# Kernel tuning notes

Hardware: AMD Instinct MI355X
Metric: run time of the kernel (lower is better)

Reference implementation:

```python
import jax, jax.numpy as jnp
import numpy as np

C_IN, C_KEY, C_VAL, C_OUT = 256, 128, 128, 256
B, H, W = 4, 64, 64
BN_EPS = 1e-5


def conv1x1(x, w, b):
    # x: [B,C,H,W], w: [O,C], b: [O]
    return jnp.einsum('bchw,oc->bohw', x, w) + b[None, :, None, None]


def bn_relu(x, gamma, beta, mean, var):
    inv = jax.lax.rsqrt(var + BN_EPS)
    y = (x - mean[None, :, None, None]) * (gamma * inv)[None, :, None, None] + beta[None, :, None, None]
    return jax.nn.relu(y)


def setup_inputs() -> dict:
    key = jax.random.key(0)
    ks = jax.random.split(key, 16)
    s = 0.05
    return {
        'x_enc': jax.random.normal(ks[0], (B, C_IN, H, W), jnp.float32),
        'x_dec': jax.random.normal(ks[1], (B, C_IN, H, W), jnp.float32),
        # f_key: conv + BN params
        'wk': jax.random.normal(ks[2], (C_KEY, C_IN), jnp.float32) * s,
        'bk': jax.random.normal(ks[3], (C_KEY,), jnp.float32) * s,
        'gk': jax.random.uniform(ks[4], (C_KEY,), jnp.float32, 0.5, 1.5),
        'betak': jax.random.normal(ks[5], (C_KEY,), jnp.float32) * s,
        'mk': jax.random.normal(ks[6], (C_KEY,), jnp.float32) * s,
        'vk': jax.random.uniform(ks[7], (C_KEY,), jnp.float32, 0.5, 1.5),
        # f_query: conv + BN params
        'wq': jax.random.normal(ks[8], (C_KEY, C_IN), jnp.float32) * s,
        'bq': jax.random.normal(ks[9], (C_KEY,), jnp.float32) * s,
        'gq': jax.random.uniform(ks[10], (C_KEY,), jnp.float32, 0.5, 1.5),
        'betaq': jax.random.normal(ks[11], (C_KEY,), jnp.float32) * s,
        'mq': jax.random.normal(ks[12], (C_KEY,), jnp.float32) * s,
        'vq': jax.random.uniform(ks[13], (C_KEY,), jnp.float32, 0.5, 1.5),
        # f_value conv
        'wv': jax.random.normal(ks[14], (C_VAL, C_IN), jnp.float32) * s,
        'bv': jnp.zeros((C_VAL,), jnp.float32),
        # output projection W (random instead of zero-init to avoid degenerate baseline)
        'wo': jax.random.normal(ks[15], (C_OUT, C_VAL), jnp.float32) * s,
        'bo': jnp.zeros((C_OUT,), jnp.float32),
    }


def reference(x_enc, x_dec, wk, bk, gk, betak, mk, vk, wq, bq, gq, betaq, mq, vq, wv, bv, wo, bo):
    b, _, h, w = x_enc.shape
    hw = h * w
    # value: [B, HW, Cv]
    value = conv1x1(x_enc, wv, bv).reshape(b, C_VAL, hw).transpose(0, 2, 1)
    # query: [B, HW, Ck]
    query = bn_relu(conv1x1(x_dec, wq, bq), gq, betaq, mq, vq).reshape(b, C_KEY, hw).transpose(0, 2, 1)
    # key: [B, Ck, HW]
    key = bn_relu(conv1x1(x_enc, wk, bk), gk, betak, mk, vk).reshape(b, C_KEY, hw)
    sim = jnp.einsum('bqc,bck->bqk', query, key) * (C_KEY ** -0.5)  # [B, HW, HW]
    attn = jax.nn.softmax(sim, axis=-1)
    context = jnp.einsum('bqk,bkc->bqc', attn, value)  # [B, HW, Cv]
    context = context.transpose(0, 2, 1).reshape(b, C_VAL, h, w)
    return conv1x1(context, wo, bo)
```

## Files before the change

kernel.cpp:

```cpp
#include <hip/hip_runtime.h>

typedef __attribute__((ext_vector_type(8))) short short8;
typedef __attribute__((ext_vector_type(4))) float floatx4;

#define HW 4096
#define CIN 256
#define CK 128
#define COUT 256
#define NB 4
#define BN_EPS 1e-5f
#define SC2 0.12751744526f

#define MFMA(a, b, c) __builtin_amdgcn_mfma_f32_16x16x32_bf16((a), (b), (c), 0, 0, 0)

__device__ __forceinline__ unsigned short f2bf(float f) {
  union { float f; unsigned u; } v; v.f = f;
  unsigned r = v.u + 0x7fffu + ((v.u >> 16) & 1u);
  return (unsigned short)(r >> 16);
}

__device__ __forceinline__ short8 pack8(const float* p) {
  short8 r;
#pragma unroll
  for (int i = 0; i < 8; ++i) r[i] = (short)f2bf(p[i]);
  return r;
}

__global__ __launch_bounds__(256) void proj_kernel(
    const float* __restrict__ x_enc, const float* __restrict__ x_dec,
    const float* __restrict__ wq, const float* __restrict__ bq,
    const float* __restrict__ gq, const float* __restrict__ betaq,
    const float* __restrict__ mq, const float* __restrict__ vq,
    const float* __restrict__ wk, const float* __restrict__ bk,
    const float* __restrict__ gk, const float* __restrict__ betak,
    const float* __restrict__ mk, const float* __restrict__ vk,
    const float* __restrict__ wv, const float* __restrict__ bv,
    unsigned short* __restrict__ Qb, unsigned short* __restrict__ Kb,
    unsigned short* __restrict__ Vt)
{
  const int tid = threadIdx.x;
  const int pt = blockIdx.x;
  const int b  = blockIdx.y;
  const int pj = blockIdx.z;

  const float* X = (pj == 0) ? x_dec : x_enc;

  __shared__ float xF[64 * 68];
  __shared__ unsigned short xT[64 * 264];

  const float* Xs = X + (size_t)b * CIN * HW + (size_t)pt * 64;
#pragma unroll
  for (int qtr = 0; qtr < 4; ++qtr) {
    if (qtr) __syncthreads();
    {
      const int c = tid >> 2;
      const int p0 = (tid & 3) * 16;
      const float* src = Xs + (size_t)(qtr * 64 + c) * HW + p0;
#pragma unroll
      for (int j = 0; j < 4; ++j)
        *(float4*)&xF[c * 68 + p0 + j * 4] = *(const float4*)(src + j * 4);
    }
    __syncthreads();
    {
      const int p = tid & 63;
      const int cb = tid >> 6;
#pragma unroll
      for (int jj = 0; jj < 2; ++jj) {
        const int c0 = (jj * 4 + cb) * 8;
        float t[8];
#pragma unroll
        for (int u = 0; u < 8; ++u) t[u] = xF[(c0 + u) * 68 + p];
        *(short8*)&xT[p * 264 + qtr * 64 + c0] = pack8(t);
      }
    }
  }
  __syncthreads();

  const int wave = tid >> 6;
  const int lane = tid & 63;
  const int lane16 = lane & 15;
  const int quad = lane >> 4;

  if (pj == 0) {
    floatx4 acc[2][4];
#pragma unroll
    for (int mt = 0; mt < 2; ++mt)
#pragma unroll
      for (int nf = 0; nf < 4; ++nf) acc[mt][nf] = (floatx4){0.f, 0.f, 0.f, 0.f};

#pragma unroll
    for (int ks = 0; ks < 8; ++ks) {
      short8 af[2];
#pragma unroll
      for (int mt = 0; mt < 2; ++mt) {
        const int o = wave * 32 + mt * 16 + lane16;
        const float* Wr = wq + (size_t)o * CIN + ks * 32 + quad * 8;
        float t[8];
        *(float4*)(t) = *(const float4*)(Wr);
        *(float4*)(t + 4) = *(const float4*)(Wr + 4);
        af[mt] = pack8(t);
      }
#pragma unroll
      for (int nf = 0; nf < 4; ++nf) {
        const short8 bf = *(const short8*)&xT[(nf * 16 + lane16) * 264 + ks * 32 + quad * 8];
#pragma unroll
        for (int mt = 0; mt < 2; ++mt) acc[mt][nf] = MFMA(af[mt], bf, acc[mt][nf]);
      }
    }

    float sc[2][4], off[2][4];
#pragma unroll
    for (int mt = 0; mt < 2; ++mt)
#pragma unroll
      for (int r = 0; r < 4; ++r) {
        const int o = wave * 32 + mt * 16 + quad * 4 + r;
        const float s = gq[o] * rsqrtf(vq[o] + BN_EPS) * SC2;
        sc[mt][r] = s;
        off[mt][r] = (bq[o] - mq[o]) * s + betaq[o] * SC2;
      }
#pragma unroll
    for (int nf = 0; nf < 4; ++nf) {
      const size_t prow = ((size_t)b * HW + pt * 64 + nf * 16 + lane16) * CK;
#pragma unroll
      for (int mt = 0; mt < 2; ++mt) {
        ushort4 pk;
        pk.x = f2bf(fmaxf(acc[mt][nf][0] * sc[mt][0] + off[mt][0], 0.f));
        pk.y = f2bf(fmaxf(acc[mt][nf][1] * sc[mt][1] + off[mt][1], 0.f));
        pk.z = f2bf(fmaxf(acc[mt][nf][2] * sc[mt][2] + off[mt][2], 0.f));
        pk.w = f2bf(fmaxf(acc[mt][nf][3] * sc[mt][3] + off[mt][3], 0.f));
        *(ushort4*)(Qb + prow + wave * 32 + mt * 16 + quad * 4) = pk;
      }
    }
  } else {
    const bool isK = (wave < 2);
    floatx4 acc[4][4];
#pragma unroll
    for (int mt = 0; mt < 4; ++mt)
#pragma unroll
      for (int nf = 0; nf < 4; ++nf) acc[mt][nf] = (floatx4){0.f, 0.f, 0.f, 0.f};

#pragma unroll
    for (int ks = 0; ks < 8; ++ks) {
      short8 af[4];
#pragma unroll
      for (int mt = 0; mt < 4; ++mt) {
        const int o = wave * 64 + mt * 16 + lane16;
        const float* Wr = (isK ? wk + (size_t)o * CIN
                               : wv + (size_t)(o - 128) * CIN) + ks * 32 + quad * 8;
        float t[8];
        *(float4*)(t) = *(const float4*)(Wr);
        *(float4*)(t + 4) = *(const float4*)(Wr + 4);
        af[mt] = pack8(t);
      }
#pragma unroll
      for (int nf = 0; nf < 4; ++nf) {
        const short8 bf = *(const short8*)&xT[(nf * 16 + lane16) * 264 + ks * 32 + quad * 8];
#pragma unroll
        for (int mt = 0; mt < 4; ++mt) acc[mt][nf] = MFMA(af[mt], bf, acc[mt][nf]);
      }
    }

    if (isK) {
      float sc[4][4], off[4][4];
#pragma unroll
      for (int mt = 0; mt < 4; ++mt)
#pragma unroll
        for (int r = 0; r < 4; ++r) {
          const int o = wave * 64 + mt * 16 + quad * 4 + r;
          const float s = gk[o] * rsqrtf(vk[o] + BN_EPS);
          sc[mt][r] = s;
          off[mt][r] = (bk[o] - mk[o]) * s + betak[o];
        }
#pragma unroll
      for (int nf = 0; nf < 4; ++nf) {
        const size_t prow = ((size_t)b * HW + pt * 64 + nf * 16 + lane16) * CK;
#pragma unroll
        for (int mt = 0; mt < 4; ++mt) {
          ushort4 pk;
          pk.x = f2bf(fmaxf(acc[mt][nf][0] * sc[mt][0] + off[mt][0], 0.f));
          pk.y = f2bf(fmaxf(acc[mt][nf][1] * sc[mt][1] + off[mt][1], 0.f));
          pk.z = f2bf(fmaxf(acc[mt][nf][2] * sc[mt][2] + off[mt][2], 0.f));
          pk.w = f2bf(fmaxf(acc[mt][nf][3] * sc[mt][3] + off[mt][3], 0.f));
          *(ushort4*)(Kb + prow + wave * 64 + mt * 16 + quad * 4) = pk;
        }
      }
    } else {
#pragma unroll
      for (int mt = 0; mt < 4; ++mt) {
#pragma unroll
        for (int r = 0; r < 4; ++r) {
          const int c = wave * 64 + mt * 16 + quad * 4 + r - 128;
          const float bias = bv[c];
          unsigned short* dst = Vt + ((size_t)(b * CK + c)) * HW + pt * 64;
#pragma unroll
          for (int nf = 0; nf < 4; ++nf)
            dst[nf * 16 + lane16] = f2bf(acc[mt][nf][r] + bias);
        }
      }
    }
  }
}

template<int NKC>
__global__ __launch_bounds__(256, 2) void attn_kernel4(
    const unsigned short* __restrict__ Qb, const unsigned short* __restrict__ Kb,
    const unsigned short* __restrict__ Vt, float* __restrict__ Opart,
    float* __restrict__ Ml)
{
  constexpr int ITERS = 64 / NKC;
  const int tid = threadIdx.x;
  const int blk = blockIdx.x;
  const int b  = blk & 3;
  const int qt = (blk >> 2) & 31;
  const int kc = blk >> 7;

  const int wave = tid >> 6;
  const int lane = tid & 63;
  const int lane16 = lane & 15;
  const int quad = lane >> 4;

  __shared__ unsigned short Kl[64 * 136];
  __shared__ unsigned short Vl[128 * 72];
  __shared__ unsigned short Pl[4][32 * 72];
  unsigned short* Pw = &Pl[wave][0];

  const int q0 = qt * 128 + wave * 32;
  short8 qf[2][4];
  {
    const unsigned short* Qs = Qb + ((size_t)b * HW + q0) * CK;
#pragma unroll
    for (int mt = 0; mt < 2; ++mt)
#pragma unroll
      for (int ks = 0; ks < 4; ++ks)
        qf[mt][ks] = *(const short8*)(Qs + (size_t)(mt * 16 + lane16) * CK + ks * 32 + quad * 8);
  }

  short8 ones;
#pragma unroll
  for (int i = 0; i < 8; ++i) ones[i] = (short)0x3F80;

  floatx4 O[2][8];
  floatx4 Lacc[2];
#pragma unroll
  for (int mt = 0; mt < 2; ++mt) {
    Lacc[mt] = (floatx4){0.f, 0.f, 0.f, 0.f};
#pragma unroll
    for (int nf = 0; nf < 8; ++nf) O[mt][nf] = (floatx4){0.f, 0.f, 0.f, 0.f};
  }

  const int krow = tid >> 4;
  const int kcol = (tid & 15) * 8;
  const int vrow = tid >> 1;
  const int vcol = (tid & 1) * 32;

  const unsigned short* Kg = Kb + (size_t)b * HW * CK + (size_t)(kc * ITERS * 64) * CK;
  const unsigned short* Vg = Vt + (size_t)b * CK * HW + kc * ITERS * 64;

  short8 kr[4], vr[4];
#pragma unroll
  for (int i2 = 0; i2 < 4; ++i2)
    kr[i2] = *(const short8*)(Kg + (size_t)(krow + i2 * 16) * CK + kcol);
#pragma unroll
  for (int i2 = 0; i2 < 4; ++i2)
    vr[i2] = *(const short8*)(Vg + (size_t)vrow * HW + vcol + i2 * 8);

  for (int it = 0; it < ITERS; ++it) {
    __syncthreads();
#pragma unroll
    for (int i2 = 0; i2 < 4; ++i2)
      *(short8*)&Kl[(krow + i2 * 16) * 136 + kcol] = kr[i2];
#pragma unroll
    for (int i2 = 0; i2 < 4; ++i2)
      *(short8*)&Vl[vrow * 72 + vcol + i2 * 8] = vr[i2];
    __syncthreads();

    if (it + 1 < ITERS) {
      const unsigned short* Kn = Kg + (size_t)((it + 1) * 64) * CK;
      const unsigned short* Vn = Vg + (it + 1) * 64;
#pragma unroll
      for (int i2 = 0; i2 < 4; ++i2)
        kr[i2] = *(const short8*)(Kn + (size_t)(krow + i2 * 16) * CK + kcol);
#pragma unroll
      for (int i2 = 0; i2 < 4; ++i2)
        vr[i2] = *(const short8*)(Vn + (size_t)vrow * HW + vcol + i2 * 8);
    }

#pragma unroll
    for (int nf = 0; nf < 4; ++nf) {
      floatx4 s0 = (floatx4){0.f, 0.f, 0.f, 0.f};
      floatx4 s1 = (floatx4){0.f, 0.f, 0.f, 0.f};
#pragma unroll
      for (int ks = 0; ks < 4; ++ks) {
        const short8 kf = *(const short8*)&Kl[(nf * 16 + lane16) * 136 + ks * 32 + quad * 8];
        s0 = MFMA(qf[0][ks], kf, s0);
        s1 = MFMA(qf[1][ks], kf, s1);
      }
#pragma unroll
      for (int r = 0; r < 4; ++r) {
        Pw[(quad * 4 + r) * 72 + nf * 16 + lane16] =
            f2bf(__builtin_amdgcn_exp2f(s0[r]));
        Pw[(16 + quad * 4 + r) * 72 + nf * 16 + lane16] =
            f2bf(__builtin_amdgcn_exp2f(s1[r]));
      }
    }
    __threadfence_block();

#pragma unroll
    for (int ks = 0; ks < 2; ++ks) {
      const short8 pf0 = *(const short8*)&Pw[lane16 * 72 + ks * 32 + quad * 8];
      const short8 pf1 = *(const short8*)&Pw[(16 + lane16) * 72 + ks * 32 + quad * 8];
      Lacc[0] = MFMA(pf0, ones, Lacc[0]);
      Lacc[1] = MFMA(pf1, ones, Lacc[1]);
#pragma unroll
      for (int nf = 0; nf < 8; ++nf) {
        const short8 vf = *(const short8*)&Vl[(nf * 16 + lane16) * 72 + ks * 32 + quad * 8];
        O[0][nf] = MFMA(pf0, vf, O[0][nf]);
        O[1][nf] = MFMA(pf1, vf, O[1][nf]);
      }
    }
  }

  const int chunk = (b * 32 + qt) * NKC + kc;
  float* Op = Opart + (size_t)chunk * (128 * 128);
#pragma unroll
  for (int mt = 0; mt < 2; ++mt)
#pragma unroll
    for (int nf = 0; nf < 8; ++nf)
#pragma unroll
      for (int r = 0; r < 4; ++r)
        Op[(size_t)(wave * 32 + mt * 16 + quad * 4 + r) * 128 + nf * 16 + lane16] = O[mt][nf][r];
  if (lane16 == 0) {
    float* Mp = Ml + (size_t)chunk * 128 + wave * 32;
#pragma unroll
    for (int mt = 0; mt < 2; ++mt)
#pragma unroll
      for (int r = 0; r < 4; ++r)
        Mp[mt * 16 + quad * 4 + r] = Lacc[mt][r];
  }
}

template<int NKC>
__global__ __launch_bounds__(256) void outproj_kernel(
    const float* __restrict__ Opart, const float* __restrict__ Ml,
    const float* __restrict__ wo, const float* __restrict__ bo,
    float* __restrict__ out)
{
  const int tid = threadIdx.x;
  const int pt = blockIdx.x;
  const int b  = blockIdx.y;
  const int wave = tid >> 6;
  const int lane = tid & 63;
  const int lane16 = lane & 15;
  const int quad = lane >> 4;

  const int qt = pt >> 2;
  const int q0 = (pt & 3) * 32;
  const int chunk0 = (b * 32 + qt) * NKC;

  float invl[2];
#pragma unroll
  for (int nf = 0; nf < 2; ++nf) {
    const int qrow = q0 + nf * 16 + lane16;
    float L = 0.f;
#pragma unroll
    for (int k = 0; k < NKC; ++k) L += Ml[(size_t)(chunk0 + k) * 128 + qrow];
    invl[nf] = 1.f / L;
  }

  floatx4 acc[4][2];
#pragma unroll
  for (int mt = 0; mt < 4; ++mt)
#pragma unroll
    for (int nf = 0; nf < 2; ++nf) acc[mt][nf] = (floatx4){0.f, 0.f, 0.f, 0.f};

#pragma unroll
  for (int ks = 0; ks < 4; ++ks) {
    short8 af[4];
#pragma unroll
    for (int mt = 0; mt < 4; ++mt) {
      const int o = wave * 64 + mt * 16 + lane16;
      const float* Wr = wo + (size_t)o * CK + ks * 32 + quad * 8;
      float t[8];
      *(float4*)(t) = *(const float4*)(Wr);
      *(float4*)(t + 4) = *(const float4*)(Wr + 4);
      af[mt] = pack8(t);
    }
#pragma unroll
    for (int nf = 0; nf < 2; ++nf) {
      const int qrow = q0 + nf * 16 + lane16;
      const float* Op = Opart + (size_t)chunk0 * 16384 + (size_t)qrow * 128 + ks * 32 + quad * 8;
      float t[8];
#pragma unroll
      for (int u = 0; u < 8; ++u) t[u] = 0.f;
#pragma unroll
      for (int k = 0; k < NKC; ++k) {
        const float4 v0 = *(const float4*)(Op + (size_t)k * 16384);
        const float4 v1 = *(const float4*)(Op + (size_t)k * 16384 + 4);
        t[0] += v0.x; t[1] += v0.y; t[2] += v0.z; t[3] += v0.w;
        t[4] += v1.x; t[5] += v1.y; t[6] += v1.z; t[7] += v1.w;
      }
      const float iv = invl[nf];
#pragma unroll
      for (int u = 0; u < 8; ++u) t[u] *= iv;
      const short8 bf = pack8(t);
#pragma unroll
      for (int mt = 0; mt < 4; ++mt) acc[mt][nf] = MFMA(af[mt], bf, acc[mt][nf]);
    }
  }

#pragma unroll
  for (int mt = 0; mt < 4; ++mt) {
#pragma unroll
    for (int r = 0; r < 4; ++r) {
      const int o = wave * 64 + mt * 16 + quad * 4 + r;
      const float bias = bo[o];
      float* dst = out + ((size_t)b * COUT + o) * HW + qt * 128 + q0;
#pragma unroll
      for (int nf = 0; nf < 2; ++nf)
        dst[nf * 16 + lane16] = acc[mt][nf][r] + bias;
    }
  }
}

extern "C" void kernel_launch(void* const* d_in, const int* in_sizes, int n_in,
                              void* d_out, int out_size, void* d_ws, size_t ws_size,
                              hipStream_t stream)
{
  (void)in_sizes; (void)n_in; (void)out_size;
  const float* x_enc = (const float*)d_in[0];
  const float* x_dec = (const float*)d_in[1];
  const float* wk    = (const float*)d_in[2];
  const float* bk    = (const float*)d_in[3];
  const float* gk    = (const float*)d_in[4];
  const float* betak = (const float*)d_in[5];
  const float* mk    = (const float*)d_in[6];
  const float* vk    = (const float*)d_in[7];
  const float* wq    = (const float*)d_in[8];
  const float* bq    = (const float*)d_in[9];
  const float* gq    = (const float*)d_in[10];
  const float* betaq = (const float*)d_in[11];
  const float* mq    = (const float*)d_in[12];
  const float* vq    = (const float*)d_in[13];
  const float* wv    = (const float*)d_in[14];
  const float* bv    = (const float*)d_in[15];
  const float* wo    = (const float*)d_in[16];
  const float* bo    = (const float*)d_in[17];
  float* out = (float*)d_out;

  const size_t qkv = (size_t)NB * HW * CK;
  unsigned short* Qb = (unsigned short*)d_ws;
  unsigned short* Kb = Qb + qkv;
  unsigned short* Vt = Kb + qkv;
  float* Opart = (float*)(Vt + qkv);
  const size_t bf16_bytes = 3 * qkv * 2;

  proj_kernel<<<dim3(64, 4, 2), 256, 0, stream>>>(
      x_enc, x_dec, wq, bq, gq, betaq, mq, vq,
      wk, bk, gk, betak, mk, vk, wv, bv, Qb, Kb, Vt);

  auto need = [&](int nkc) {
    return bf16_bytes + (size_t)128 * nkc * (16384 + 128) * sizeof(float);
  };
  if (ws_size >= need(4)) {
    float* Ml = Opart + (size_t)128 * 4 * 16384;
    attn_kernel4<4><<<dim3(512), 256, 0, stream>>>(Qb, Kb, Vt, Opart, Ml);
    outproj_kernel<4><<<dim3(128, 4), 256, 0, stream>>>(Opart, Ml, wo, bo, out);
  } else if (ws_size >= need(2)) {
    float* Ml = Opart + (size_t)128 * 2 * 16384;
    attn_kernel4<2><<<dim3(256), 256, 0, stream>>>(Qb, Kb, Vt, Opart, Ml);
    outproj_kernel<2><<<dim3(128, 4), 256, 0, stream>>>(Opart, Ml, wo, bo, out);
  } else {
    float* Ml = Opart + (size_t)128 * 1 * 16384;
    attn_kernel4<1><<<dim3(128), 256, 0, stream>>>(Qb, Kb, Vt, Opart, Ml);
    outproj_kernel<1><<<dim3(128, 4), 256, 0, stream>>>(Opart, Ml, wo, bo, out);
  }
}
```

Before: 192.5 us.

## Pre-pack weights to bf16 MFMA layout, add 8-way key split, restage outproj

A new prep kernel converts wq, wk/wv and wo once per call into bf16 fragments laid out in MFMA operand order. The projection and output kernels then load these packed fragments directly instead of converting fp32 weights in every block. The output projection now reduces the partial attention outputs into a shared-memory tile over 16 query rows, which avoids redundant reductions. A new 8-way key-chunk split is tried first when workspace allows. This adds one extra launch and more partial-output traffic when the 8-way split is used.

Result: faster. 177.4 us (-7.8%).

```diff
diff --git a/kernel.cpp b/kernel.cpp
--- a/kernel.cpp
+++ b/kernel.cpp
@@ -26,15 +26,53 @@
   return r;
 }
 
+__global__ __launch_bounds__(256) void prep_kernel(
+    const float* __restrict__ wq, const float* __restrict__ wk,
+    const float* __restrict__ wv, const float* __restrict__ wo,
+    unsigned short* __restrict__ WqP, unsigned short* __restrict__ WkvP,
+    unsigned short* __restrict__ WoP)
+{
+  const int t = blockIdx.x * 256 + threadIdx.x;
+  float tmp[8];
+  if (t < 4096) {
+    const int lane = t & 63, mt = (t >> 6) & 1, wave = (t >> 7) & 3, ks = t >> 9;
+    const int lane16 = lane & 15, quad = lane >> 4;
+    const int o = wave * 32 + mt * 16 + lane16;
+    const float* src = wq + (size_t)o * CIN + ks * 32 + quad * 8;
+    *(float4*)tmp = *(const float4*)src;
+    *(float4*)(tmp + 4) = *(const float4*)(src + 4);
+    *(short8*)&WqP[(size_t)t * 8] = pack8(tmp);
+  } else if (t < 12288) {
+    const int u = t - 4096;
+    const int lane = u & 63, mt = (u >> 6) & 3, wave = (u >> 8) & 3, ks = u >> 10;
+    const int lane16 = lane & 15, quad = lane >> 4;
+    const int o = wave * 64 + mt * 16 + lane16;
+    const float* row = (o < 128) ? wk + (size_t)o * CIN : wv + (size_t)(o - 128) * CIN;
+    const float* src = row + ks * 32 + quad * 8;
+    *(float4*)tmp = *(const float4*)src;
+    *(float4*)(tmp + 4) = *(const float4*)(src + 4);
+    *(short8*)&WkvP[(size_t)u * 8] = pack8(tmp);
+  } else {
+    const int u = t - 12288;
+    const int lane = u & 63, mt = (u >> 6) & 3, wave = (u >> 8) & 3, ks = u >> 10;
+    const int lane16 = lane & 15, quad = lane >> 4;
+    const int o = wave * 64 + mt * 16 + lane16;
+    const float* src = wo + (size_t)o * CK + ks * 32 + quad * 8;
+    *(float4*)tmp = *(const float4*)src;
+    *(float4*)(tmp + 4) = *(const float4*)(src + 4);
+    *(short8*)&WoP[(size_t)u * 8] = pack8(tmp);
+  }
+}
+
 __global__ __launch_bounds__(256) void proj_kernel(
     const float* __restrict__ x_enc, const float* __restrict__ x_dec,
-    const float* __restrict__ wq, const float* __restrict__ bq,
-    const float* __restrict__ gq, const float* __restrict__ betaq,
-    const float* __restrict__ mq, const float* __restrict__ vq,
-    const float* __restrict__ wk, const float* __restrict__ bk,
-    const float* __restrict__ gk, const float* __restrict__ betak,
-    const float* __restrict__ mk, const float* __restrict__ vk,
-    const float* __restrict__ wv, const float* __restrict__ bv,
+    const unsigned short* __restrict__ WqP, const unsigned short* __restrict__ WkvP,
+    const float* __restrict__ bq, const float* __restrict__ gq,
+    const float* __restrict__ betaq, const float* __restrict__ mq,
+    const float* __restrict__ vq,
+    const float* __restrict__ bk, const float* __restrict__ gk,
+    const float* __restrict__ betak, const float* __restrict__ mk,
+    const float* __restrict__ vk, const float* __restrict__ bv,
     unsigned short* __restrict__ Qb, unsigned short* __restrict__ Kb,
     unsigned short* __restrict__ Vt)
 {
@@ -92,14 +130,8 @@
     for (int ks = 0; ks < 8; ++ks) {
       short8 af[2];
 #pragma unroll
-      for (int mt = 0; mt < 2; ++mt) {
-        const int o = wave * 32 + mt * 16 + lane16;
-        const float* Wr = wq + (size_t)o * CIN + ks * 32 + quad * 8;
-        float t[8];
-        *(float4*)(t) = *(const float4*)(Wr);
-        *(float4*)(t + 4) = *(const float4*)(Wr + 4);
-        af[mt] = pack8(t);
-      }
+      for (int mt = 0; mt < 2; ++mt)
+        af[mt] = *(const short8*)&WqP[(size_t)((((ks * 4 + wave) * 2 + mt) * 64) + lane) * 8];
 #pragma unroll
       for (int nf = 0; nf < 4; ++nf) {
         const short8 bf = *(const short8*)&xT[(nf * 16 + lane16) * 264 + ks * 32 + quad * 8];
@@ -143,15 +175,8 @@
     for (int ks = 0; ks < 8; ++ks) {
       short8 af[4];
 #pragma unroll
-      for (int mt = 0; mt < 4; ++mt) {
-        const int o = wave * 64 + mt * 16 + lane16;
-        const float* Wr = (isK ? wk + (size_t)o * CIN
-                               : wv + (size_t)(o - 128) * CIN) + ks * 32 + quad * 8;
-        float t[8];
-        *(float4*)(t) = *(const float4*)(Wr);
-        *(float4*)(t + 4) = *(const float4*)(Wr + 4);
-        af[mt] = pack8(t);
-      }
+      for (int mt = 0; mt < 4; ++mt)
+        af[mt] = *(const short8*)&WkvP[(size_t)((((ks * 4 + wave) * 4 + mt) * 64) + lane) * 8];
 #pragma unroll
       for (int nf = 0; nf < 4; ++nf) {
         const short8 bf = *(const short8*)&xT[(nf * 16 + lane16) * 264 + ks * 32 + quad * 8];
@@ -202,7 +227,7 @@
 }
 
 template<int NKC>
-__global__ __launch_bounds__(256, 2) void attn_kernel4(
+__global__ __launch_bounds__(256, 2) void attn_kernel5(
     const unsigned short* __restrict__ Qb, const unsigned short* __restrict__ Kb,
     const unsigned short* __restrict__ Vt, float* __restrict__ Opart,
     float* __restrict__ Ml)
@@ -342,69 +367,58 @@
 template<int NKC>
 __global__ __launch_bounds__(256) void outproj_kernel(
     const float* __restrict__ Opart, const float* __restrict__ Ml,
-    const float* __restrict__ wo, const float* __restrict__ bo,
+    const unsigned short* __restrict__ WoP, const float* __restrict__ bo,
     float* __restrict__ out)
 {
   const int tid = threadIdx.x;
   const int pt = blockIdx.x;
   const int b  = blockIdx.y;
+  const int qt = pt >> 3;
+  const int q0 = (pt & 7) * 16;
+  const int chunk0 = (b * 32 + qt) * NKC;
+
+  __shared__ unsigned short Ctile[16 * 136];
+
+  {
+    const int row = tid >> 4;
+    const int c8  = (tid & 15) * 8;
+    float L = 0.f;
+#pragma unroll
+    for (int k = 0; k < NKC; ++k) L += Ml[(size_t)(chunk0 + k) * 128 + q0 + row];
+    float acc[8];
+#pragma unroll
+    for (int i = 0; i < 8; ++i) acc[i] = 0.f;
+#pragma unroll
+    for (int k = 0; k < NKC; ++k) {
+      const float* Op = Opart + (size_t)(chunk0 + k) * 16384 + (size_t)(q0 + row) * 128 + c8;
+      const float4 v0 = *(const float4*)(Op);
+      const float4 v1 = *(const float4*)(Op + 4);
+      acc[0] += v0.x; acc[1] += v0.y; acc[2] += v0.z; acc[3] += v0.w;
+      acc[4] += v1.x; acc[5] += v1.y; acc[6] += v1.z; acc[7] += v1.w;
+    }
+    const float inv = 1.f / L;
+#pragma unroll
+    for (int i = 0; i < 8; ++i) acc[i] *= inv;
+    *(short8*)&Ctile[row * 136 + c8] = pack8(acc);
+  }
+  __syncthreads();
+
   const int wave = tid >> 6;
   const int lane = tid & 63;
   const int lane16 = lane & 15;
   const int quad = lane >> 4;
 
-  const int qt = pt >> 2;
-  const int q0 = (pt & 3) * 32;
-  const int chunk0 = (b * 32 + qt) * NKC;
-
-  float invl[2];
-#pragma unroll
-  for (int nf = 0; nf < 2; ++nf) {
-    const int qrow = q0 + nf * 16 + lane16;
-    float L = 0.f;
-#pragma unroll
-    for (int k = 0; k < NKC; ++k) L += Ml[(size_t)(chunk0 + k) * 128 + qrow];
-    invl[nf] = 1.f / L;
-  }
-
-  floatx4 acc[4][2];
-#pragma unroll
-  for (int mt = 0; mt < 4; ++mt)
-#pragma unroll
-    for (int nf = 0; nf < 2; ++nf) acc[mt][nf] = (floatx4){0.f, 0.f, 0.f, 0.f};
+  floatx4 acc[4];
+#pragma unroll
+  for (int mt = 0; mt < 4; ++mt) acc[mt] = (floatx4){0.f, 0.f, 0.f, 0.f};
 
 #pragma unroll
   for (int ks = 0; ks < 4; ++ks) {
-    short8 af[4];
+    const short8 bf = *(const short8*)&Ctile[lane16 * 136 + ks * 32 + quad * 8];
 #pragma unroll
     for (int mt = 0; mt < 4; ++mt) {
-      const int o = wave * 64 + mt * 16 + lane16;
-      const float* Wr = wo + (size_t)o * CK + ks * 32 + quad * 8;
-      float t[8];
-      *(float4*)(t) = *(const float4*)(Wr);
-      *(float4*)(t + 4) = *(const float4*)(Wr + 4);
-      af[mt] = pack8(t);
-    }
-#pragma unroll
-    for (int nf = 0; nf < 2; ++nf) {
-      const int qrow = q0 + nf * 16 + lane16;
-      const float* Op = Opart + (size_t)chunk0 * 16384 + (size_t)qrow * 128 + ks * 32 + quad * 8;
-      float t[8];
-#pragma unroll
-      for (int u = 0; u < 8; ++u) t[u] = 0.f;
-#pragma unroll
-      for (int k = 0; k < NKC; ++k) {
-        const float4 v0 = *(const float4*)(Op + (size_t)k * 16384);
-        const float4 v1 = *(const float4*)(Op + (size_t)k * 16384 + 4);
-        t[0] += v0.x; t[1] += v0.y; t[2] += v0.z; t[3] += v0.w;
-        t[4] += v1.x; t[5] += v1.y; t[6] += v1.z; t[7] += v1.w;
-      }
-      const float iv = invl[nf];
-#pragma unroll
-      for (int u = 0; u < 8; ++u) t[u] *= iv;
-      const short8 bf = pack8(t);
-#pragma unroll
-      for (int mt = 0; mt < 4; ++mt) acc[mt][nf] = MFMA(af[mt], bf, acc[mt][nf]);
+      const short8 af = *(const short8*)&WoP[(size_t)((((ks * 4 + wave) * 4 + mt) * 64) + lane) * 8];
+      acc[mt] = MFMA(af, bf, acc[mt]);
     }
   }
 
@@ -413,11 +427,8 @@
 #pragma unroll
     for (int r = 0; r < 4; ++r) {
       const int o = wave * 64 + mt * 16 + quad * 4 + r;
-      const float bias = bo[o];
       float* dst = out + ((size_t)b * COUT + o) * HW + qt * 128 + q0;
-#pragma unroll
-      for (int nf = 0; nf < 2; ++nf)
-        dst[nf * 16 + lane16] = acc[mt][nf][r] + bias;
+      dst[lane16] = acc[mt][r] + bo[o];
     }
   }
 }
@@ -448,30 +459,38 @@
   float* out = (float*)d_out;
 
   const size_t qkv = (size_t)NB * HW * CK;
-  unsigned short* Qb = (unsigned short*)d_ws;
-  unsigned short* Kb = Qb + qkv;
-  unsigned short* Vt = Kb + qkv;
+  unsigned short* WqP  = (unsigned short*)d_ws;
+  unsigned short* WkvP = WqP + 32768;
+  unsigned short* WoP  = WkvP + 65536;
+  unsigned short* Qb   = WoP + 32768;
+  unsigned short* Kb   = Qb + qkv;
+  unsigned short* Vt   = Kb + qkv;
   float* Opart = (float*)(Vt + qkv);
-  const size_t bf16_bytes = 3 * qkv * 2;
-
+  const size_t fixed_bytes = 131072 * 2 + 3 * qkv * 2;
+
+  prep_kernel<<<dim3(64), 256, 0, stream>>>(wq, wk, wv, wo, WqP, WkvP, WoP);
   proj_kernel<<<dim3(64, 4, 2), 256, 0, stream>>>(
-      x_enc, x_dec, wq, bq, gq, betaq, mq, vq,
-      wk, bk, gk, betak, mk, vk, wv, bv, Qb, Kb, Vt);
+      x_enc, x_dec, WqP, WkvP,
+      bq, gq, betaq, mq, vq, bk, gk, betak, mk, vk, bv, Qb, Kb, Vt);
 
   auto need = [&](int nkc) {
-    return bf16_bytes + (size_t)128 * nkc * (16384 + 128) * sizeof(float);
+    return fixed_bytes + (size_t)128 * nkc * (16384 + 128) * sizeof(float);
   };
-  if (ws_size >= need(4)) {
+  if (ws_size >= need(8)) {
+    float* Ml = Opart + (size_t)128 * 8 * 16384;
+    attn_kernel5<8><<<dim3(1024), 256, 0, stream>>>(Qb, Kb, Vt, Opart, Ml);
+    outproj_kernel<8><<<dim3(256, 4), 256, 0, stream>>>(Opart, Ml, WoP, bo, out);
+  } else if (ws_size >= need(4)) {
     float* Ml = Opart + (size_t)128 * 4 * 16384;
-    attn_kernel4<4><<<dim3(512), 256, 0, stream>>>(Qb, Kb, Vt, Opart, Ml);
-    outproj_kernel<4><<<dim3(128, 4), 256, 0, stream>>>(Opart, Ml, wo, bo, out);
+    attn_kernel5<4><<<dim3(512), 256, 0, stream>>>(Qb, Kb, Vt, Opart, Ml);
+    outproj_kernel<4><<<dim3(256, 4), 256, 0, stream>>>(Opart, Ml, WoP, bo, out);
   } else if (ws_size >= need(2)) {
     float* Ml = Opart + (size_t)128 * 2 * 16384;
-    attn_kernel4<2><<<dim3(256), 256, 0, stream>>>(Qb, Kb, Vt, Opart, Ml);
-    outproj_kernel<2><<<dim3(128, 4), 256, 0, stream>>>(Opart, Ml, wo, bo, out);
+    attn_kernel5<2><<<dim3(256), 256, 0, stream>>>(Qb, Kb, Vt, Opart, Ml);
+    outproj_kernel<2><<<dim3(256, 4), 256, 0, stream>>>(Opart, Ml, WoP, bo, out);
   } else {
     float* Ml = Opart + (size_t)128 * 1 * 16384;
-    attn_kernel4<1><<<dim3(128), 256, 0, stream>>>(Qb, Kb, Vt, Opart, Ml);
-    outproj_kernel<1><<<dim3(128, 4), 256, 0, stream>>>(Opart, Ml, wo, bo, out);
-  }
-}
+    attn_kernel5<1><<<dim3(128), 256, 0, stream>>>(Qb, Kb, Vt, Opart, Ml);
+    outproj_kernel<1><<<dim3(256, 4), 256, 0, stream>>>(Opart, Ml, WoP, bo, out);
+  }
+}
```
